# Performance work log

Hardware: AMD Instinct MI355X
Metric: run time of the kernel (lower is better)

## Reference

```python
import jax, jax.numpy as jnp
import numpy as np

N = 20000
E = 640000
F_IN = 128
C_T = 8
L_T = 10 * N
HEADS = 8
HDIM = 64
NEG_SLOPE = 0.2


def setup_inputs() -> dict:
    key = jax.random.key(0)
    ks = jax.random.split(key, 20)
    d = {}
    d["x"] = jax.random.normal(ks[0], (N, F_IN), dtype=jnp.float32)
    d["edge_index"] = jax.random.randint(ks[1], (2, E), 0, N, dtype=jnp.int64)
    d["temporal"] = jax.random.normal(ks[2], (C_T, L_T), dtype=jnp.float32)
    # GCNConv(F_IN, 16)
    d["W1"] = jax.random.normal(ks[3], (F_IN, 16), dtype=jnp.float32) * 0.1
    d["b1"] = jnp.zeros((16,), dtype=jnp.float32)
    # GATConv(16, 64, heads=8), concat -> 512
    d["W2"] = jax.random.normal(ks[4], (16, HEADS * HDIM), dtype=jnp.float32) * 0.1
    d["att_src"] = jax.random.normal(ks[5], (HEADS, HDIM), dtype=jnp.float32) * 0.1
    d["att_dst"] = jax.random.normal(ks[6], (HEADS, HDIM), dtype=jnp.float32) * 0.1
    d["b2"] = jnp.zeros((HEADS * HDIM,), dtype=jnp.float32)
    # TemporalCNN
    d["cw1"] = jax.random.normal(ks[7], (32, C_T, 3), dtype=jnp.float32) * 0.1
    d["cb1"] = jnp.zeros((32,), dtype=jnp.float32)
    d["cw2"] = jax.random.normal(ks[8], (64, 32, 3), dtype=jnp.float32) * 0.05
    d["cb2"] = jnp.zeros((64,), dtype=jnp.float32)
    d["cw3"] = jax.random.normal(ks[9], (128, 64, 3), dtype=jnp.float32) * 0.05
    d["cb3"] = jnp.zeros((128,), dtype=jnp.float32)
    d["fw1"] = jax.random.normal(ks[10], (256, 128 * 10), dtype=jnp.float32) * 0.02
    d["fb1"] = jnp.zeros((256,), dtype=jnp.float32)
    d["fw2"] = jax.random.normal(ks[11], (64, 256), dtype=jnp.float32) * 0.05
    d["fb2"] = jnp.zeros((64,), dtype=jnp.float32)
    return d


def _conv1d(x, w, b):
    # x: [1, C, L], w: [O, C, 3]; padding=1 == SAME for k=3
    out = jax.lax.conv_general_dilated(
        x, w, window_strides=(1,), padding="SAME",
        dimension_numbers=("NCH", "OIH", "NCH"))
    return out + b[None, :, None]


def _gcn(x, src, dst, W, b):
    # PyG GCNConv: add self-loops, symmetric normalization
    h = x @ W                                   # [N, 16]
    deg = jax.ops.segment_sum(jnp.ones_like(dst, dtype=h.dtype), dst, num_segments=N)
    dinv = jax.lax.rsqrt(jnp.maximum(deg, 1.0))
    norm = dinv[src] * dinv[dst]                # [E+N]
    out = jax.ops.segment_sum(h[src] * norm[:, None], dst, num_segments=N)
    return out + b


def _gat(x, src, dst, W, att_src, att_dst, b):
    h = (x @ W).reshape(N, HEADS, HDIM)         # [N, 8, 64]
    a_s = jnp.einsum("nhd,hd->nh", h, att_src)  # [N, 8]
    a_d = jnp.einsum("nhd,hd->nh", h, att_dst)
    e = a_s[src] + a_d[dst]                     # [E+N, 8], message j->i: src=j, dst=i
    e = jnp.where(e >= 0, e, NEG_SLOPE * e)     # LeakyReLU(0.2)
    # segment softmax over incoming edges of each dst node
    m = jax.ops.segment_max(e, dst, num_segments=N)
    m = jnp.where(jnp.isfinite(m), m, 0.0)
    ex = jnp.exp(e - m[dst])
    s = jax.ops.segment_sum(ex, dst, num_segments=N)
    alpha = ex / (s[dst] + 1e-16)               # [E+N, 8]
    out = jax.ops.segment_sum(h[src] * alpha[:, :, None], dst, num_segments=N)
    return out.reshape(N, HEADS * HDIM) + b


def reference(x, edge_index, temporal, W1, b1, W2, att_src, att_dst, b2,
              cw1, cb1, cw2, cb2, cw3, cb3, fw1, fb1, fw2, fb2):
    # ---- graph branch ----
    loops = jnp.arange(N, dtype=edge_index.dtype)
    src = jnp.concatenate([edge_index[0], loops])
    dst = jnp.concatenate([edge_index[1], loops])
    g = _gcn(x, src, dst, W1, b1)
    g = jax.nn.relu(g)
    # F.dropout with training=False (eval) -> identity
    x1 = _gat(g, src, dst, W2, att_src, att_dst, b2)   # [N, 512]
    # ---- temporal branch ----
    t = temporal[None]                                  # [1, C, L]
    t = jax.nn.relu(_conv1d(t, cw1, cb1))
    t = jax.nn.relu(_conv1d(t, cw2, cb2))
    t = jax.nn.relu(_conv1d(t, cw3, cb3))               # [1, 128, L]
    t = t.reshape(-1, 128 * 10)                         # [N, 1280] (same as torch .view)
    t = jax.nn.relu(t @ fw1.T + fb1)
    x2 = t @ fw2.T + fb2                                # [N, 64]
    return jnp.concatenate([x1, x2], axis=1)            # [N, 576]
```

## Files before the change

kernel.cpp:

```cpp
#include <hip/hip_runtime.h>
#include <hip/hip_bf16.h>

#define NN 20000
#define EE 640000
#define FIN 128
#define CT 8
#define LT 200000
#define HEADS 8
#define HDIM 64
#define F1 16
#define F2 512
#define OUTF 576

typedef short s16x8 __attribute__((ext_vector_type(8)));
typedef float f32x4 __attribute__((ext_vector_type(4)));

static __device__ __forceinline__ unsigned f2bf_bits(float x) {
  unsigned u = __float_as_uint(x);
  return (u + 0x7fffu + ((u >> 16) & 1u)) >> 16;
}

static __device__ __forceinline__ void gl16(const void* g, void* l) {
  __builtin_amdgcn_global_load_lds(
      (const __attribute__((address_space(1))) unsigned*)g,
      (__attribute__((address_space(3))) unsigned*)l, 16, 0, 0);
}


static __device__ void dev_prep_all(
    int b, int t, const float* __restrict__ cw1, float* __restrict__ wt1,
    const float* __restrict__ cw2, short* __restrict__ wb2,
    const float* __restrict__ cw3, short* __restrict__ wb3,
    const float* __restrict__ W2, const float* __restrict__ asrc,
    const float* __restrict__ adst, float* __restrict__ WS, float* __restrict__ WD) {
  if (b < 3) {
    int i = b * 256 + t;
    if (i < 32 * 8 * 3) {
      int o = i / 24, r = i % 24;
      int c = r / 3, k = r % 3;
      wt1[(c * 3 + k) * 32 + o] = cw1[i];
    }
  } else if (b < 27) {
    int i = (b - 3) * 256 + t;
    int o = i / 96, r = i % 96;
    int ic = r / 3, kk = r % 3;
    wb2[o * 96 + kk * 32 + ic] = (short)f2bf_bits(cw2[i]);
  } else if (b < 123) {
    int i = (b - 27) * 256 + t;
    int o = i / 192, r = i % 192;
    int ic = r / 3, kk = r % 3;
    wb3[o * 192 + kk * 64 + ic] = (short)f2bf_bits(cw3[i]);
  } else {
    int k = (t & 127) >> 3, h = t & 7;
    const float* av = (t < 128) ? asrc : adst;
    float acc = 0.f;
    for (int d = 0; d < 64; d++) acc += W2[k * F2 + h * 64 + d] * av[h * 64 + d];
    ((t < 128) ? WS : WD)[k * 8 + h] = acc;
  }
}

static __device__ void dev_conv_fast(
    char* smp, int b, int t, const float* __restrict__ in,
    __hip_bfloat16* __restrict__ out, const float* __restrict__ wt,
    const float* __restrict__ bias) {
  constexpr int C = 8, O = 32, P = 4, OCG = O / 2;
  float (*tile)[68] = (float(*)[68])smp;
  __hip_bfloat16 (*ot)[66] = (__hip_bfloat16(*)[66])(smp + 2176);
  int ocg = t % OCG;
  int pg = t / OCG;
  long base = (long)b * 64;

  for (int i = t; i < C * 66; i += 256) {
    int c = i / 66, p = i % 66;
    long l = base + p - 1;
    tile[c][p] = (l >= 0 && l < LT) ? in[(long)c * LT + l] : 0.f;
  }
  __syncthreads();

  int oc0 = 2 * ocg;
  int p0 = pg * P;
  float acc[2][P];
#pragma unroll
  for (int j = 0; j < 2; j++)
#pragma unroll
    for (int p = 0; p < P; p++) acc[j][p] = 0.f;

  for (int ic = 0; ic < C; ic++) {
    float x[P + 2];
#pragma unroll
    for (int q = 0; q < P / 4; q++) {
      float4 v = *(const float4*)&tile[ic][p0 + 4 * q];
      x[4 * q] = v.x; x[4 * q + 1] = v.y; x[4 * q + 2] = v.z; x[4 * q + 3] = v.w;
    }
    {
      float2 v = *(const float2*)&tile[ic][p0 + P];
      x[P] = v.x; x[P + 1] = v.y;
    }
    const float* wrow = wt + (long)ic * 3 * O;
    float wv[3][2];
#pragma unroll
    for (int kk = 0; kk < 3; kk++) {
      float2 w2 = *(const float2*)&wrow[kk * O + oc0];
      wv[kk][0] = w2.x; wv[kk][1] = w2.y;
    }
#pragma unroll
    for (int kk = 0; kk < 3; kk++)
#pragma unroll
      for (int j = 0; j < 2; j++)
#pragma unroll
        for (int p = 0; p < P; p++) acc[j][p] += x[p + kk] * wv[kk][j];
  }
  float b0 = bias[oc0], b1 = bias[oc0 + 1];
#pragma unroll
  for (int p = 0; p < P; p++) {
    ot[oc0][p0 + p] = __float2bfloat16(fmaxf(acc[0][p] + b0, 0.f));
    ot[oc0 + 1][p0 + p] = __float2bfloat16(fmaxf(acc[1][p] + b1, 0.f));
  }
  __syncthreads();
  for (int i = t; i < O * 32; i += 256) {
    int oc = i >> 5, pp = i & 31;
    unsigned v = ((const unsigned*)&ot[oc][0])[pp];
    *(unsigned*)&out[(long)oc * LT + base + 2 * pp] = v;
  }
}

template <int C, int O, int MPW>
static __device__ void dev_conv_mfma(
    char* smp, int b, int t, const short* __restrict__ in,
    short* __restrict__ out, const short* __restrict__ w,
    const float* __restrict__ bias) {
  constexpr int K = 3 * C;
  constexpr int NS = K / 32;
  constexpr int XP = C + 8;
  constexpr int OP = 132;
  short* xT = (short*)smp;
  long base = (long)b * 128;

  if (base >= 2 && base + 131 < LT) {
    for (int idx = t; idx < C * 67; idx += 256) {
      int ic = idx / 67, q = idx % 67;
      unsigned v = *(const unsigned*)(in + (long)ic * LT + base + 2 * q - 2);
      int p0 = 2 * q - 1;
      if (q > 0) xT[p0 * XP + ic] = (short)(v & 0xffffu);
      if (q < 66) xT[(p0 + 1) * XP + ic] = (short)(v >> 16);
    }
  } else {
    for (int idx = t; idx < C * 132; idx += 256) {
      int ic = idx / 132, p = idx % 132;
      long l = base + p - 1;
      xT[p * XP + ic] = (l >= 0 && l < LT) ? in[(long)ic * LT + l] : (short)0;
    }
  }
  __syncthreads();

  int wave = t >> 6, lane = t & 63;
  int n = lane & 15, kg = lane >> 4;
  int m0 = wave * (MPW * 16);

  f32x4 acc[MPW][8] = {};
#pragma unroll
  for (int s = 0; s < NS; s++) {
    const int kk = (s * 32) / C;
    const int ic0 = (s * 32) % C + kg * 8;
    s16x8 a[MPW];
#pragma unroll
    for (int mi = 0; mi < MPW; mi++)
      a[mi] = *(const s16x8*)(w + (long)(m0 + mi * 16 + n) * K + s * 32 + kg * 8);
#pragma unroll
    for (int nt = 0; nt < 8; nt++) {
      s16x8 bb = *(const s16x8*)(xT + (nt * 16 + n + kk) * XP + ic0);
#pragma unroll
      for (int mi = 0; mi < MPW; mi++)
        acc[mi][nt] = __builtin_amdgcn_mfma_f32_16x16x32_bf16(a[mi], bb, acc[mi][nt], 0, 0, 0);
    }
  }

  __syncthreads();
  short* ob = (short*)smp;
#pragma unroll
  for (int mi = 0; mi < MPW; mi++) {
    int o = m0 + mi * 16 + kg * 4;
#pragma unroll
    for (int nt = 0; nt < 8; nt++) {
      int p = nt * 16 + n;
#pragma unroll
      for (int r = 0; r < 4; r++) {
        float v = fmaxf(acc[mi][nt][r] + bias[o + r], 0.f);
        ob[(o + r) * OP + p] = (short)f2bf_bits(v);
      }
    }
  }
  __syncthreads();
  const unsigned* obu = (const unsigned*)smp;
  for (int idx = t; idx < O * 64; idx += 256) {
    int o = idx >> 6, q = idx & 63;
    long l = base + 2 * q;
    if (l < LT)
      *(unsigned*)(out + (long)o * LT + l) = obu[o * (OP / 2) + q];
  }
}

static __device__ void dev_scan(
    char* smp, int t, const int* __restrict__ deg, int* __restrict__ offs,
    float* __restrict__ dinv) {
  int* sums = (int*)smp;
  const int CH = 79;
  int base = t * CH;
  int s = 0;
  for (int i = 0; i < CH; i++) {
    int idx = base + i;
    if (idx < NN) s += deg[idx] + 1;
  }
  sums[t] = s;
  __syncthreads();
  for (int off = 1; off < 256; off <<= 1) {
    int v = (t >= off) ? sums[t - off] : 0;
    __syncthreads();
    sums[t] += v;
    __syncthreads();
  }
  int run = (t > 0) ? sums[t - 1] : 0;
  for (int i = 0; i < CH; i++) {
    int idx = base + i;
    if (idx < NN) {
      int d = deg[idx];
      offs[idx] = run;
      dinv[idx] = rsqrtf((float)(d + 1));
      run += d + 1;
    }
  }
  if (t == 255) offs[NN] = sums[255];
}

static __device__ void dev_fill(
    int b, int t, const int* __restrict__ src, const int* __restrict__ dst,
    const int* __restrict__ offs, int* __restrict__ cursor, int* __restrict__ csr) {
  int e = b * 256 + t;
  if (e < EE) {
    int d = dst[e];
    int pos = atomicAdd(&cursor[d], 1);
    csr[offs[d] + pos] = src[e];
  } else if (e < EE + NN) {
    int i = e - EE;
    int pos = atomicAdd(&cursor[i], 1);
    csr[offs[i] + pos] = i;
  }
}

static __device__ void dev_h1(
    char* smp, int b, int t, const float* __restrict__ x,
    const float* __restrict__ W1, const float* __restrict__ dinv,
    float* __restrict__ h1s) {
  float* ws = (float*)smp;
  float* xs = (float*)(smp + 8192);
  int i0 = b * 16;
  for (int i = t; i < 512; i += 256)
    *(float4*)&ws[4 * i] = *(const float4*)&W1[4 * i];
  for (int i = t; i < 512; i += 256) {
    int nl = i >> 5, q = i & 31;
    *(float4*)&xs[nl * 132 + 4 * q] = *(const float4*)&x[(long)(i0 + nl) * FIN + 4 * q];
  }
  __syncthreads();
  int nl = t >> 4, f = t & 15;
  float acc = 0.f;
#pragma unroll 8
  for (int k = 0; k < FIN; k++) acc += xs[nl * 132 + k] * ws[k * 16 + f];
  int n = i0 + nl;
  h1s[n * F1 + f] = acc * dinv[n];
}

static __device__ void dev_fwprep(
    int b, int t, const float* __restrict__ fw1, __hip_bfloat16* __restrict__ w1b,
    const float* __restrict__ fw2, float* __restrict__ fw2t) {
  if (b < 1280) {
    int i = b * 256 + t;
    w1b[i] = __float2bfloat16(fw1[i]);
  } else {
    int i = (b - 1280) * 256 + t;
    int o = i / 256, j = i % 256;
    fw2t[j * 64 + o] = fw2[i];
  }
}

static __device__ void dev_fc1(
    char* smp, int bid, int t, const __hip_bfloat16* __restrict__ t3,
    const __hip_bfloat16* __restrict__ w, const float* __restrict__ fb1,
    float* __restrict__ out) {
  short* As = (short*)smp;
  short* Bs = (short*)(smp + 16384);
  int wid = t >> 6, lane = t & 63;
  int bn = bid & 1, bm = bid >> 1;
  int mrow = lane & 15, kg = lane >> 4;

  const char* tb = (const char*)t3;
  const char* wb = (const char*)w;
  int u0 = wid * 128 + lane;
  int u1 = u0 + 64;
  int ra0 = u0 >> 2, ca0 = u0 & 3;
  int ra1 = u1 >> 2, ca1 = u1 & 3;
  long ga0 = ((long)min(bm * 128 + ra0, NN - 1) * 1280 + ca0 * 8) * 2;
  long ga1 = ((long)min(bm * 128 + ra1, NN - 1) * 1280 + ca1 * 8) * 2;
  long gb0 = ((long)(bn * 128 + ra0) * 1280 + ca0 * 8) * 2;
  long gb1 = ((long)(bn * 128 + ra1) * 1280 + ca1 * 8) * 2;
  int l0 = (wid * 2 + 0) * 512;
  int l1 = (wid * 2 + 1) * 512;

  auto stage = [&](int buf, int k0) {
    long kb = (long)k0 * 2;
    gl16(tb + ga0 + kb, As + buf * 4096 + l0);
    gl16(tb + ga1 + kb, As + buf * 4096 + l1);
    gl16(wb + gb0 + kb, Bs + buf * 4096 + l0);
    gl16(wb + gb1 + kb, Bs + buf * 4096 + l1);
  };

  stage(0, 0);
  __syncthreads();

  int wr = wid >> 1, wc = wid & 1;
  f32x4 acc[4][4] = {};
  for (int s = 0; s < 40; s++) {
    int buf = s & 1;
    if (s + 1 < 40) stage(buf ^ 1, (s + 1) * 32);
    s16x8 a[4], bb[4];
#pragma unroll
    for (int mi = 0; mi < 4; mi++)
      a[mi] = *(const s16x8*)&As[buf * 4096 + (wr * 64 + mi * 16 + mrow) * 32 + kg * 8];
#pragma unroll
    for (int ni = 0; ni < 4; ni++)
      bb[ni] = *(const s16x8*)&Bs[buf * 4096 + (wc * 64 + ni * 16 + mrow) * 32 + kg * 8];
#pragma unroll
    for (int mi = 0; mi < 4; mi++)
#pragma unroll
      for (int ni = 0; ni < 4; ni++)
        acc[mi][ni] = __builtin_amdgcn_mfma_f32_16x16x32_bf16(a[mi], bb[ni], acc[mi][ni], 0, 0, 0);
    __syncthreads();
  }

  int node_base = bm * 128 + wr * 64 + kg * 4;
  int col_base = bn * 128 + wc * 64 + mrow;
#pragma unroll
  for (int ni = 0; ni < 4; ni++) {
    int col = col_base + ni * 16;
    float bias = fb1[col];
#pragma unroll
    for (int mi = 0; mi < 4; mi++) {
      int node = node_base + mi * 16;
#pragma unroll
      for (int r = 0; r < 4; r++) {
        if (node + r < NN)
          out[(long)(node + r) * 256 + col] = fmaxf(acc[mi][ni][r] + bias, 0.f);
      }
    }
  }
}

static __device__ void dev_gcn(
    int b, int t, const float* __restrict__ h1s, const int* __restrict__ offs,
    const int* __restrict__ csr, const float* __restrict__ dinv,
    const float* __restrict__ b1, float* __restrict__ g) {
  int wave = t >> 6;
  int lane = t & 63;
  int i = b * 4 + wave;
  int f = lane & 15, grp = lane >> 4;
  int beg = offs[i], end = offs[i + 1];
  float acc = 0.f;
  for (int idx = beg + grp; idx < end; idx += 4)
    acc += h1s[csr[idx] * F1 + f];
  acc += __shfl_down(acc, 32);
  acc += __shfl_down(acc, 16);
  if (lane < 16) g[i * F1 + f] = fmaxf(acc * dinv[i] + b1[f], 0.f);
}

static __device__ void dev_fc2(
    char* smp, int b, int t, const float* __restrict__ fc1o,
    const float* __restrict__ fw2t, const float* __restrict__ fb2,
    float* __restrict__ out) {
  float* sh = (float*)smp;
  int m0 = b * 16;
  for (int i = t; i < 1024; i += 256) {
    int nd = i >> 6, q = i & 63;
    *(float4*)&sh[nd * 260 + 4 * q] = *(const float4*)&fc1o[(long)(m0 + nd) * 256 + 4 * q];
  }
  __syncthreads();
  int wave = t >> 6, o = t & 63;
  int nb = wave * 4;
  float acc[4];
  float bias = fb2[o];
#pragma unroll
  for (int i = 0; i < 4; i++) acc[i] = bias;
  for (int j = 0; j < 256; j++) {
    float wv = fw2t[j * 64 + o];
#pragma unroll
    for (int i = 0; i < 4; i++) acc[i] += sh[(nb + i) * 260 + j] * wv;
  }
#pragma unroll
  for (int i = 0; i < 4; i++)
    out[(long)(m0 + nb + i) * OUTF + F2 + o] = acc[i];
}

static __device__ void dev_h2att(
    char* smp, int b, int t, const float* __restrict__ g,
    const float* __restrict__ W2, const float* __restrict__ WS,
    const float* __restrict__ WD, unsigned* __restrict__ h2hm,
    float* __restrict__ AS, float* __restrict__ AD) {
  float* glb = (float*)smp;
  int i0 = b * 32;
  for (int idx = t; idx < 512; idx += 256)
    glb[(idx >> 4) * 20 + (idx & 15)] = g[i0 * 16 + idx];
  __syncthreads();

  int f0 = 2 * t;
  int h = t >> 5, c32 = t & 31;
  float w0[16], w1[16];
#pragma unroll
  for (int k = 0; k < 16; k++) {
    float2 wv = *(const float2*)&W2[k * F2 + f0];
    w0[k] = wv.x; w1[k] = wv.y;
  }
  for (int nl = 0; nl < 32; nl++) {
    float a0 = 0.f, a1 = 0.f;
#pragma unroll
    for (int kk = 0; kk < 4; kk++) {
      f32x4 gv = *(const f32x4*)&glb[nl * 20 + 4 * kk];
#pragma unroll
      for (int r = 0; r < 4; r++) {
        a0 += gv[r] * w0[4 * kk + r];
        a1 += gv[r] * w1[4 * kk + r];
      }
    }
    h2hm[((long)h * NN + i0 + nl) * 32 + c32] = f2bf_bits(a0) | (f2bf_bits(a1) << 16);
  }
  int nl = t >> 3, hh = t & 7;
  float s = 0.f, d = 0.f;
#pragma unroll
  for (int k = 0; k < 16; k++) {
    float gv = glb[nl * 20 + k];
    s += gv * WS[k * 8 + hh];
    d += gv * WD[k * 8 + hh];
  }
  AS[(long)hh * NN + i0 + nl] = s;
  AD[(long)hh * NN + i0 + nl] = d;
}


__global__ __launch_bounds__(256) void k_prep(
    const float* cw1, float* wt1, const float* cw2, short* wb2,
    const float* cw3, short* wb3, const float* W2, const float* asrc,
    const float* adst, float* WS, float* WD, int* zbase) {
  int b = blockIdx.x, t = threadIdx.x;
  if (b < 124) dev_prep_all(b, t, cw1, wt1, cw2, wb2, cw3, wb3, W2, asrc, adst, WS, WD);
  else {
    int i = (b - 124) * 256 + t;
    if (i < 40000) zbase[i] = 0;
  }
}

__global__ __launch_bounds__(256) void k_conv1_deg(
    const float* temporal, __hip_bfloat16* T1b, const float* wt1, const float* cb1,
    const int* e_dst, int* deg) {
  extern __shared__ char smem[];
  int b = blockIdx.x;
  if (b < 3125) dev_conv_fast(smem, b, threadIdx.x, temporal, T1b, wt1, cb1);
  else {
    int e = (b - 3125) * 256 + threadIdx.x;
    if (e < EE) atomicAdd(&deg[e_dst[e]], 1);
  }
}

__global__ __launch_bounds__(256) void k_conv2_scan(
    const short* T1b, short* T2b, const short* wb2, const float* cb2,
    const int* deg, int* offs, float* dinv,
    const float* fw1, __hip_bfloat16* w1b, const float* fw2, float* fw2t) {
  extern __shared__ char smem[];
  int b = blockIdx.x;
  if (b < 1563) dev_conv_mfma<32, 64, 1>(smem, b, threadIdx.x, T1b, T2b, wb2, cb2);
  else if (b == 1563) dev_scan(smem, threadIdx.x, deg, offs, dinv);
  else dev_fwprep(b - 1564, threadIdx.x, fw1, w1b, fw2, fw2t);
}

__global__ __launch_bounds__(256) void k_conv3_misc(
    const short* T2b, short* T3b, const short* wb3, const float* cb3,
    const int* e_src, const int* e_dst, const int* offs, int* cursor, int* csr,
    const float* x, const float* W1, const float* dinv, float* h1s) {
  extern __shared__ char smem[];
  int b = blockIdx.x, t = threadIdx.x;
  if (b < 1563) dev_conv_mfma<64, 128, 2>(smem, b, t, T2b, T3b, wb3, cb3);
  else if (b < 4142) dev_fill(b - 1563, t, e_src, e_dst, offs, cursor, csr);
  else dev_h1(smem, b - 4142, t, x, W1, dinv, h1s);
}

__global__ __launch_bounds__(256) void k_fc1_gcn(
    const __hip_bfloat16* t3, const __hip_bfloat16* w, const float* fb1, float* fc1o,
    const float* h1s, const int* offs, const int* csr, const float* dinv,
    const float* b1, float* g) {
  extern __shared__ char smem[];
  int b = blockIdx.x, t = threadIdx.x;
  if (b < 314) dev_fc1(smem, b, t, t3, w, fb1, fc1o);
  else dev_gcn(b - 314, t, h1s, offs, csr, dinv, b1, g);
}

__global__ __launch_bounds__(256) void k_fc2_h2att(
    const float* fc1o, const float* fw2t, const float* fb2, float* out,
    const float* g, const float* W2, const float* WS, const float* WD,
    unsigned* h2hm, float* AS, float* AD) {
  extern __shared__ char smem[];
  int b = blockIdx.x, t = threadIdx.x;
  if (b < 1250) dev_fc2(smem, b, t, fc1o, fw2t, fb2, out);
  else dev_h2att(smem, b - 1250, t, g, W2, WS, WD, h2hm, AS, AD);
}

__global__ __launch_bounds__(256) void gat_fused_kernel(
    const unsigned* __restrict__ h2hm, const float* __restrict__ AS,
    const float* __restrict__ AD, const int* __restrict__ offs,
    const int* __restrict__ csr, const float* __restrict__ b2,
    float* __restrict__ out) {
  __shared__ __align__(16) unsigned long long pairs[4][64];
  __shared__ __align__(16) float accb[4][8][68];
  int h = blockIdx.x & 7;
  int gn = blockIdx.x >> 3;
  int wave = threadIdx.x >> 6;
  int lane = threadIdx.x & 63;
  int i = gn * 4 + wave;
  int beg = offs[i], end = offs[i + 1];
  const float* ASh = AS + (long)h * NN;
  float ad = AD[(long)h * NN + i];
  const char* hb2 = (const char*)(h2hm + (long)h * NN * 32);
  int octet = lane >> 3, q = lane & 7;
  unsigned laneoff = (unsigned)q * 16u;
  unsigned long long* prs = &pairs[wave][0];

  float acc[8] = {0.f, 0.f, 0.f, 0.f, 0.f, 0.f, 0.f, 0.f};
  float sum = 0.f;

  for (int c = beg; c < end; c += 64) {
    int cnt = end - c;
    if (cnt > 64) cnt = 64;
    unsigned off = 0u;
    float ex = 0.f;
    if (lane < cnt) {
      int s = csr[c + lane];
      float e = ASh[s] + ad;
      e = (e >= 0.f) ? e : 0.2f * e;
      ex = __expf(e);
      sum += ex;
      off = (unsigned)s << 7;
    }
    asm volatile("" ::: "memory");
    prs[lane] = ((unsigned long long)__float_as_uint(ex) << 32) | off;
    asm volatile("" ::: "memory");
    int nj = (cnt + 7) >> 3;
    const unsigned long long* pp = prs + octet;
#pragma unroll 2
    for (int j = 0; j < nj; j++) {
      unsigned long long pr = pp[(long)j * 8];
      unsigned voff = (unsigned)pr | laneoff;
      float aj = __uint_as_float((unsigned)(pr >> 32));
      uint4 v = *(const uint4*)(hb2 + voff);
      acc[0] += __uint_as_float(v.x << 16) * aj;
      acc[1] += __uint_as_float(v.x & 0xffff0000u) * aj;
      acc[2] += __uint_as_float(v.y << 16) * aj;
      acc[3] += __uint_as_float(v.y & 0xffff0000u) * aj;
      acc[4] += __uint_as_float(v.z << 16) * aj;
      acc[5] += __uint_as_float(v.z & 0xffff0000u) * aj;
      acc[6] += __uint_as_float(v.w << 16) * aj;
      acc[7] += __uint_as_float(v.w & 0xffff0000u) * aj;
    }
    asm volatile("" ::: "memory");
  }
#pragma unroll
  for (int o = 32; o > 0; o >>= 1) sum += __shfl_xor(sum, o, 64);
  float rinv = 1.f / (sum + 1e-16f);
  float* ab = &accb[wave][octet][q * 8];
  f32x4 lo = {acc[0], acc[1], acc[2], acc[3]};
  f32x4 hi = {acc[4], acc[5], acc[6], acc[7]};
  *(f32x4*)ab = lo;
  *(f32x4*)(ab + 4) = hi;
  asm volatile("" ::: "memory");
  float r = 0.f;
#pragma unroll
  for (int o = 0; o < 8; o++) r += accb[wave][o][lane];
  out[(long)i * OUTF + h * 64 + lane] = r * rinv + b2[h * 64 + lane];
}


extern "C" void kernel_launch(void* const* d_in, const int* in_sizes, int n_in,
                              void* d_out, int out_size, void* d_ws, size_t ws_size,
                              hipStream_t stream) {
  const float* x        = (const float*)d_in[0];
  const int*   eidx     = (const int*)d_in[1];
  const float* temporal = (const float*)d_in[2];
  const float* W1       = (const float*)d_in[3];
  const float* b1       = (const float*)d_in[4];
  const float* W2       = (const float*)d_in[5];
  const float* att_src  = (const float*)d_in[6];
  const float* att_dst  = (const float*)d_in[7];
  const float* b2       = (const float*)d_in[8];
  const float* cw1      = (const float*)d_in[9];
  const float* cb1      = (const float*)d_in[10];
  const float* cw2      = (const float*)d_in[11];
  const float* cb2      = (const float*)d_in[12];
  const float* cw3      = (const float*)d_in[13];
  const float* cb3      = (const float*)d_in[14];
  const float* fw1      = (const float*)d_in[15];
  const float* fb1      = (const float*)d_in[16];
  const float* fw2      = (const float*)d_in[17];
  const float* fb2      = (const float*)d_in[18];
  float* out = (float*)d_out;

  const int* e_src = eidx;
  const int* e_dst = eidx + EE;

  char* ws = (char*)d_ws;
  int*   CURSOR = (int*)  (ws + 0);
  int*   DEG    = (int*)  (ws + 80000);
  int*   OFFS   = (int*)  (ws + 160000);
  float* DINV   = (float*)(ws + 240128);
  int*   CSR    = (int*)  (ws + 320128);
  float* H1S    = (float*)(ws + 2960128);
  float* G      = (float*)(ws + 4240128);
  float* AS     = (float*)(ws + 5520128);
  float* AD     = (float*)(ws + 6160128);
  __hip_bfloat16* T2b = (__hip_bfloat16*)(ws + 6800128);
  float* FC1OUT = (float*)(ws + 6800128);
  __hip_bfloat16* T1b = (__hip_bfloat16*)(ws + 32400128);
  unsigned* H2HM = (unsigned*)(ws + 32400128);
  __hip_bfloat16* T3b = (__hip_bfloat16*)(ws + 32400128);
  __hip_bfloat16* FW1BF = (__hip_bfloat16*)(ws + 83600128);
  float* FW2T = (float*)(ws + 84255488);
  float* WT1 = out;
  short* WB2 = (short*)((char*)d_out + 3072);
  short* WB3 = (short*)((char*)d_out + 15360);
  float* WSM = (float*)((char*)d_out + 64512);
  float* WDM = (float*)((char*)d_out + 65024);

  k_prep<<<281, 256, 0, stream>>>(cw1, WT1, cw2, WB2, cw3, WB3,
                                  W2, att_src, att_dst, WSM, WDM, (int*)ws);
  k_conv1_deg<<<5625, 256, 6400, stream>>>(temporal, T1b, WT1, cb1, e_dst, DEG);
  k_conv2_scan<<<2908, 256, 16896, stream>>>((const short*)T1b, (short*)T2b, WB2, cb2,
                                             DEG, OFFS, DINV,
                                             fw1, FW1BF, fw2, FW2T);
  k_conv3_misc<<<5392, 256, 33792, stream>>>((const short*)T2b, (short*)T3b, WB3, cb3,
                                             e_src, e_dst, OFFS, CURSOR, CSR,
                                             x, W1, DINV, H1S);
  k_fc1_gcn<<<5314, 256, 32768, stream>>>(T3b, FW1BF, fb1, FC1OUT,
                                          H1S, OFFS, CSR, DINV, b1, G);
  k_fc2_h2att<<<1875, 256, 16640, stream>>>(FC1OUT, FW2T, fb2, out,
                                            G, W2, WSM, WDM, H2HM, AS, AD);
  gat_fused_kernel<<<(NN / 4) * 8, 256, 0, stream>>>(H2HM, AS, AD, OFFS, CSR, b2, out);
}
```

Measured before the change: 425.2 us.

## Rebalance graph-prep work across conv kernels and move zeroing to memset

Zeroing of the degree/cursor buffers moves to a hipMemsetAsync, and the degree atomics move into the prep kernel. The scan now runs alongside conv1, and CSR fill, h1 and fw prep run alongside conv2, leaving conv3 as a standalone kernel. This shifts the graph preprocessing earlier in the stage sequence so the per-launch work is better balanced. The cost is an extra memset launch and a conv3 launch that no longer has other work to overlap with.

Measured after the change: 447.1 us. 1.05x slower.

```diff
diff --git a/kernel.cpp b/kernel.cpp
--- a/kernel.cpp
+++ b/kernel.cpp
@@ -443,50 +443,44 @@
 }
 
 
-__global__ __launch_bounds__(256) void k_prep(
+__global__ __launch_bounds__(256) void k_prep_deg(
     const float* cw1, float* wt1, const float* cw2, short* wb2,
     const float* cw3, short* wb3, const float* W2, const float* asrc,
-    const float* adst, float* WS, float* WD, int* zbase) {
+    const float* adst, float* WS, float* WD, const int* e_dst, int* deg) {
   int b = blockIdx.x, t = threadIdx.x;
   if (b < 124) dev_prep_all(b, t, cw1, wt1, cw2, wb2, cw3, wb3, W2, asrc, adst, WS, WD);
   else {
-    int i = (b - 124) * 256 + t;
-    if (i < 40000) zbase[i] = 0;
-  }
-}
-
-__global__ __launch_bounds__(256) void k_conv1_deg(
+    int e = (b - 124) * 256 + t;
+    if (e < EE) atomicAdd(&deg[e_dst[e]], 1);
+  }
+}
+
+__global__ __launch_bounds__(256) void k_conv1_scan(
     const float* temporal, __hip_bfloat16* T1b, const float* wt1, const float* cb1,
-    const int* e_dst, int* deg) {
+    const int* deg, int* offs, float* dinv) {
   extern __shared__ char smem[];
   int b = blockIdx.x;
   if (b < 3125) dev_conv_fast(smem, b, threadIdx.x, temporal, T1b, wt1, cb1);
-  else {
-    int e = (b - 3125) * 256 + threadIdx.x;
-    if (e < EE) atomicAdd(&deg[e_dst[e]], 1);
-  }
-}
-
-__global__ __launch_bounds__(256) void k_conv2_scan(
+  else dev_scan(smem, threadIdx.x, deg, offs, dinv);
+}
+
+__global__ __launch_bounds__(256) void k_conv2_misc(
     const short* T1b, short* T2b, const short* wb2, const float* cb2,
-    const int* deg, int* offs, float* dinv,
+    const int* e_src, const int* e_dst, const int* offs, int* cursor, int* csr,
+    const float* x, const float* W1, const float* dinv, float* h1s,
     const float* fw1, __hip_bfloat16* w1b, const float* fw2, float* fw2t) {
   extern __shared__ char smem[];
-  int b = blockIdx.x;
-  if (b < 1563) dev_conv_mfma<32, 64, 1>(smem, b, threadIdx.x, T1b, T2b, wb2, cb2);
-  else if (b == 1563) dev_scan(smem, threadIdx.x, deg, offs, dinv);
-  else dev_fwprep(b - 1564, threadIdx.x, fw1, w1b, fw2, fw2t);
-}
-
-__global__ __launch_bounds__(256) void k_conv3_misc(
-    const short* T2b, short* T3b, const short* wb3, const float* cb3,
-    const int* e_src, const int* e_dst, const int* offs, int* cursor, int* csr,
-    const float* x, const float* W1, const float* dinv, float* h1s) {
+  int b = blockIdx.x, t = threadIdx.x;
+  if (b < 1563) dev_conv_mfma<32, 64, 1>(smem, b, t, T1b, T2b, wb2, cb2);
+  else if (b < 4142) dev_fill(b - 1563, t, e_src, e_dst, offs, cursor, csr);
+  else if (b < 5392) dev_h1(smem, b - 4142, t, x, W1, dinv, h1s);
+  else dev_fwprep(b - 5392, t, fw1, w1b, fw2, fw2t);
+}
+
+__global__ __launch_bounds__(256) void k_conv3(
+    const short* T2b, short* T3b, const short* wb3, const float* cb3) {
   extern __shared__ char smem[];
-  int b = blockIdx.x, t = threadIdx.x;
-  if (b < 1563) dev_conv_mfma<64, 128, 2>(smem, b, t, T2b, T3b, wb3, cb3);
-  else if (b < 4142) dev_fill(b - 1563, t, e_src, e_dst, offs, cursor, csr);
-  else dev_h1(smem, b - 4142, t, x, W1, dinv, h1s);
+  dev_conv_mfma<64, 128, 2>(smem, blockIdx.x, threadIdx.x, T2b, T3b, wb3, cb3);
 }
 
 __global__ __launch_bounds__(256) void k_fc1_gcn(
@@ -633,15 +627,16 @@
   float* WSM = (float*)((char*)d_out + 64512);
   float* WDM = (float*)((char*)d_out + 65024);
 
-  k_prep<<<281, 256, 0, stream>>>(cw1, WT1, cw2, WB2, cw3, WB3,
-                                  W2, att_src, att_dst, WSM, WDM, (int*)ws);
-  k_conv1_deg<<<5625, 256, 6400, stream>>>(temporal, T1b, WT1, cb1, e_dst, DEG);
-  k_conv2_scan<<<2908, 256, 16896, stream>>>((const short*)T1b, (short*)T2b, WB2, cb2,
-                                             DEG, OFFS, DINV,
+  hipMemsetAsync(ws, 0, 160000, stream);
+  k_prep_deg<<<2624, 256, 0, stream>>>(cw1, WT1, cw2, WB2, cw3, WB3,
+                                       W2, att_src, att_dst, WSM, WDM, e_dst, DEG);
+  k_conv1_scan<<<3126, 256, 6400, stream>>>(temporal, T1b, WT1, cb1,
+                                            DEG, OFFS, DINV);
+  k_conv2_misc<<<6736, 256, 16896, stream>>>((const short*)T1b, (short*)T2b, WB2, cb2,
+                                             e_src, e_dst, OFFS, CURSOR, CSR,
+                                             x, W1, DINV, H1S,
                                              fw1, FW1BF, fw2, FW2T);
-  k_conv3_misc<<<5392, 256, 33792, stream>>>((const short*)T2b, (short*)T3b, WB3, cb3,
-                                             e_src, e_dst, OFFS, CURSOR, CSR,
-                                             x, W1, DINV, H1S);
+  k_conv3<<<1563, 256, 33792, stream>>>((const short*)T2b, (short*)T3b, WB3, cb3);
   k_fc1_gcn<<<5314, 256, 32768, stream>>>(T3b, FW1BF, fb1, FC1OUT,
                                           H1S, OFFS, CSR, DINV, b1, G);
   k_fc2_h2att<<<1875, 256, 16640, stream>>>(FC1OUT, FW2T, fb2, out,
```
